# Performance work log

Hardware: AMD Instinct MI355X
Metric: run time of the kernel (lower is better)

## Reference

```python
import jax, jax.numpy as jnp
import numpy as np

DIM = 1024
HEADS = 16
DIM_HEAD = 64
INNER = HEADS * DIM_HEAD  # 1024
MLP = 4096
NQ = 16384
NW = 1024
LN_EPS = 1e-5
L2_EPS = 1e-12


def setup_inputs() -> dict:
    key = jax.random.key(0)
    ks = jax.random.split(key, 12)
    s = 0.02
    return {
        "queries": jax.random.normal(ks[0], (NQ, DIM), jnp.float32),
        "prototypes": jax.random.normal(ks[1], (NW, DIM), jnp.float32),
        "ln1_w": 1.0 + s * jax.random.normal(ks[2], (DIM,), jnp.float32),
        "ln1_b": s * jax.random.normal(ks[3], (DIM,), jnp.float32),
        "wq": s * jax.random.normal(ks[4], (DIM, INNER), jnp.float32),
        "wk": s * jax.random.normal(ks[5], (DIM, INNER), jnp.float32),
        "wv": s * jax.random.normal(ks[6], (DIM, INNER), jnp.float32),
        "wo": s * jax.random.normal(ks[7], (INNER, DIM), jnp.float32),
        "bo": jnp.zeros((DIM,), jnp.float32),
        "ln2_w": 1.0 + s * jax.random.normal(ks[8], (DIM,), jnp.float32),
        "ln2_b": s * jax.random.normal(ks[9], (DIM,), jnp.float32),
        "w1": s * jax.random.normal(ks[10], (DIM, MLP), jnp.float32),
        "b1": jnp.zeros((MLP,), jnp.float32),
        "w2": s * jax.random.normal(ks[11], (MLP, DIM), jnp.float32),
        "b2": jnp.zeros((DIM,), jnp.float32),
    }


def _layernorm(x, w, b):
    mu = jnp.mean(x, axis=-1, keepdims=True)
    var = jnp.mean(jnp.square(x - mu), axis=-1, keepdims=True)
    return (x - mu) * jax.lax.rsqrt(var + LN_EPS) * w + b


def _l2norm(x):
    n = jnp.sqrt(jnp.sum(jnp.square(x), axis=-1, keepdims=True))
    return x / jnp.maximum(n, L2_EPS)


def reference(queries, prototypes, ln1_w, ln1_b, wq, wk, wv, wo, bo,
              ln2_w, ln2_b, w1, b1, w2, b2):
    residual = queries
    qn = _layernorm(queries, ln1_w, ln1_b)
    pn = _layernorm(prototypes, ln1_w, ln1_b)
    # projections -> (h, q, d) / (h, n, d)
    q = (qn @ wq).reshape(NQ, HEADS, DIM_HEAD).transpose(1, 0, 2)
    k = (pn @ wk).reshape(NW, HEADS, DIM_HEAD).transpose(1, 0, 2)
    v = (pn @ wv).reshape(NW, HEADS, DIM_HEAD).transpose(1, 0, 2)
    attn = jnp.einsum('hqd,hnd->hqn', _l2norm(q), _l2norm(k))  # cosine, no softmax
    out = jnp.einsum('hqn,hnd->hqd', attn, v)
    out = out.transpose(1, 0, 2).reshape(NQ, INNER)
    out = out @ wo + bo + residual
    residual2 = out
    h = _layernorm(out, ln2_w, ln2_b)
    h = jax.nn.gelu(h @ w1 + b1, approximate=False) @ w2 + b2
    return h + residual2
```

## Files before the change

### kernel.cpp

```cpp
#include <hip/hip_runtime.h>
#include <hip/hip_bf16.h>

typedef _Float16 f16;
typedef __attribute__((ext_vector_type(8))) _Float16 f16x8;
typedef __attribute__((ext_vector_type(4))) _Float16 f16x4;
typedef __attribute__((ext_vector_type(4))) float f32x4;

#define DIM 1024
#define HEADS 16
#define DHEAD 64
#define MLPD 4096
#define NQ 16384
#define NW 1024
#define MCHUNK 32

#define WAITV(n) asm volatile("s_waitcnt vmcnt(" #n ")" ::: "memory")
#define WAITL0 asm volatile("s_waitcnt lgkmcnt(0)" ::: "memory")

__device__ __forceinline__ void glds16(const f16* g, f16* l) {
  __builtin_amdgcn_global_load_lds(
      (const __attribute__((address_space(1))) void*)g,
      (__attribute__((address_space(3))) void*)l, 16, 0, 0);
}

__global__ __launch_bounds__(256) void ln_f16_k(
    const float* __restrict__ X, const float* __restrict__ w,
    const float* __restrict__ b, f16* __restrict__ O) {
  const int row = blockIdx.x;
  const int t = threadIdx.x;
  const float4 v = ((const float4*)(X + (long)row * DIM))[t];
  float s = v.x + v.y + v.z + v.w;
  float s2 = v.x * v.x + v.y * v.y + v.z * v.z + v.w * v.w;
#pragma unroll
  for (int m = 1; m < 64; m <<= 1) {
    s += __shfl_xor(s, m);
    s2 += __shfl_xor(s2, m);
  }
  __shared__ float ps[4], ps2[4];
  const int lane = t & 63, wid = t >> 6;
  if (lane == 0) { ps[wid] = s; ps2[wid] = s2; }
  __syncthreads();
  s = ps[0] + ps[1] + ps[2] + ps[3];
  s2 = ps2[0] + ps2[1] + ps2[2] + ps2[3];
  const float mu = s * (1.0f / DIM);
  const float inv = rsqrtf(s2 * (1.0f / DIM) - mu * mu + 1e-5f);
  const float4 wv = ((const float4*)w)[t];
  const float4 bv = ((const float4*)b)[t];
  f16x4 o;
  o[0] = (f16)((v.x - mu) * inv * wv.x + bv.x);
  o[1] = (f16)((v.y - mu) * inv * wv.y + bv.y);
  o[2] = (f16)((v.z - mu) * inv * wv.z + bv.z);
  o[3] = (f16)((v.w - mu) * inv * wv.w + bv.w);
  *(f16x4*)(O + (long)row * DIM + t * 4) = o;
}

__global__ __launch_bounds__(256) void tcast_k(const float* __restrict__ X,
                                               f16* __restrict__ O, int R, int C) {
  __shared__ float tile[32][33];
  const int c0 = blockIdx.x * 32, r0 = blockIdx.y * 32;
  const int tx = threadIdx.x, ty = threadIdx.y;
#pragma unroll
  for (int j = 0; j < 4; ++j)
    tile[ty + j * 8][tx] = X[(long)(r0 + ty + j * 8) * C + c0 + tx];
  __syncthreads();
#pragma unroll
  for (int j = 0; j < 4; ++j)
    O[(long)(c0 + ty + j * 8) * R + r0 + tx] = (f16)tile[tx][ty + j * 8];
}

__global__ __launch_bounds__(256) void calc_m_part_k(const f16* __restrict__ kh,
                                                     const f16* __restrict__ v,
                                                     float* __restrict__ Mp) {
  const int h = blockIdx.x, ch = blockIdx.y;
  const int t = threadIdx.x;
  const int d1 = t >> 2;
  const int d2b = (t & 3) * 16;
  float acc[16] = {};
  const int n0 = ch * (NW / MCHUNK);
#pragma unroll 4
  for (int n = n0; n < n0 + NW / MCHUNK; ++n) {
    const float kv = (float)kh[(long)n * DIM + h * DHEAD + d1];
    const f16x8* vp = (const f16x8*)&v[(long)n * DIM + h * DHEAD + d2b];
    const f16x8 v0 = vp[0], v1 = vp[1];
#pragma unroll
    for (int j = 0; j < 8; ++j) acc[j] += kv * (float)v0[j];
#pragma unroll
    for (int j = 0; j < 8; ++j) acc[8 + j] += kv * (float)v1[j];
  }
  float* o = &Mp[((long)(h * MCHUNK + ch)) * 4096 + d1 * 64 + d2b];
#pragma unroll
  for (int j = 0; j < 16; ++j) o[j] = acc[j];
}

__global__ __launch_bounds__(256) void calc_m_reduce_k(const float* __restrict__ Mp,
                                                       float* __restrict__ Mo) {
  const int h = blockIdx.x;
  const int t = threadIdx.x;
#pragma unroll
  for (int e = t; e < 4096; e += 256) {
    float s = 0.f;
#pragma unroll
    for (int c = 0; c < MCHUNK; ++c)
      s += Mp[((long)(h * MCHUNK + c)) * 4096 + e];
    Mo[h * 4096 + e] = s;
  }
}

__global__ __launch_bounds__(256) void calc_wefft_k(const float* __restrict__ M,
                                                    const float* __restrict__ wo,
                                                    f16* __restrict__ Wt) {
  const int h = blockIdx.x, jt = blockIdx.y;
  const int t = threadIdx.x;
  const int jl = t & 63;
  const int il0 = (t >> 6) * 16;
  const int j = jt * 64 + jl;
  float acc[16] = {};
  for (int d = 0; d < DHEAD; ++d) {
    const float w = wo[(long)(h * DHEAD + d) * DIM + j];
    const float* mrow = &M[h * 4096 + il0 * 64 + d];
#pragma unroll
    for (int r = 0; r < 16; ++r) acc[r] += mrow[r * 64] * w;
  }
#pragma unroll
  for (int r = 0; r < 16; ++r)
    Wt[(long)j * DIM + h * DHEAD + il0 + r] = (f16)acc[r];
}

enum {
  EPI_F16 = 0,
  EPI_L2N = 1,
  EPI_BIAS_RES = 2,
  EPI_GELU = 3
};

template <int EPI>
__global__ __launch_bounds__(512, 2) void gemm256(
    const f16* __restrict__ A, const f16* __restrict__ Bt, int M, int N, int K,
    const float* __restrict__ bias, const float* resid, void* out) {
  __shared__ __align__(16) f16 lds[3 * 16384];

  const int tid = threadIdx.x;
  const int lane = tid & 63;
  const int wid = tid >> 6;
  const int wm = wid >> 2;
  const int wn = wid & 3;

  int bm, bn;
  {
    const int total = gridDim.x * gridDim.y;
    const int orig = blockIdx.y * gridDim.x + blockIdx.x;
    int swz = orig;
    if ((total & 7) == 0) swz = (orig & 7) * (total >> 3) + (orig >> 3);
    bm = swz % gridDim.x;
    bn = swz / gridDim.x;
  }

  const int srow = tid >> 2;
  const int scol = (((tid & 3) ^ ((tid >> 3) & 3))) * 8;
  const f16* agp = A + (long)(bm * 256 + srow) * K + scol;
  const f16* bgp = Bt + (long)(bn * 256 + srow) * K + scol;
  const long h128 = (long)128 * K;

  auto STAGE = [&](int c, int t) {
    const long go = (long)t * 32;
    f16* base = &lds[c * 16384 + tid * 8];
    glds16(agp + go, base);
    glds16(agp + h128 + go, base + 4096);
    glds16(bgp + go, base + 8192);
    glds16(bgp + h128 + go, base + 12288);
  };

  const int NT = K >> 5;
  STAGE(0, 0);
  STAGE(1, 1);
  STAGE(2, 2);
  WAITV(8);
  __builtin_amdgcn_s_barrier();

  const int l15 = lane & 15;
  const int kA = ((lane >> 4) * 8) ^ (((lane >> 1) & 3) * 8);
  const int abase = (wm * 128 + l15) * 32 + kA;
  const int bbase = (wn * 64 + l15) * 32 + kA;

  f32x4 acc[8][4] = {};

  for (int t = 0; t < NT; ++t) {
    const int c = t % 3;
    const f16* Ab = &lds[c * 16384];
    const f16* Bb = Ab + 8192;
    f16x8 a[8], b[4];
#pragma unroll
    for (int mi = 0; mi < 8; ++mi)
      a[mi] = *(const f16x8*)&Ab[abase + mi * 512];
#pragma unroll
    for (int nj = 0; nj < 4; ++nj)
      b[nj] = *(const f16x8*)&Bb[bbase + nj * 512];
    WAITL0;
    __builtin_amdgcn_sched_barrier(0);
    __builtin_amdgcn_s_barrier();
    if (t + 3 < NT) STAGE(c, t + 3);
    __builtin_amdgcn_s_setprio(1);
#pragma unroll
    for (int mi = 0; mi < 8; ++mi)
#pragma unroll
      for (int nj = 0; nj < 4; ++nj)
        acc[mi][nj] = __builtin_amdgcn_mfma_f32_16x16x32_f16(a[mi], b[nj],
                                                             acc[mi][nj], 0, 0, 0);
    __builtin_amdgcn_s_setprio(0);
    if (t + 4 <= NT) WAITV(8);
    else if (t + 3 == NT) WAITV(4);
    else if (t + 2 == NT) WAITV(0);
    __builtin_amdgcn_s_barrier();
  }

  const int r0 = bm * 256 + wm * 128;
  const int c0 = bn * 256 + wn * 64;
  const int lr = (lane >> 4) * 4;
  const int lc = l15;

#pragma unroll
  for (int mi = 0; mi < 8; ++mi) {
#pragma unroll
    for (int i = 0; i < 4; ++i) {
      const long r = r0 + mi * 16 + lr + i;
      if (EPI == EPI_L2N) {
        float ss = 0.f;
#pragma unroll
        for (int nj = 0; nj < 4; ++nj) {
          const float x = acc[mi][nj][i];
          ss += x * x;
        }
        ss += __shfl_xor(ss, 1);
        ss += __shfl_xor(ss, 2);
        ss += __shfl_xor(ss, 4);
        ss += __shfl_xor(ss, 8);
        const float inv = 1.0f / fmaxf(sqrtf(ss), 1e-12f);
#pragma unroll
        for (int nj = 0; nj < 4; ++nj)
          ((f16*)out)[r * N + c0 + nj * 16 + lc] = (f16)(acc[mi][nj][i] * inv);
      } else if (EPI == EPI_F16) {
#pragma unroll
        for (int nj = 0; nj < 4; ++nj)
          ((f16*)out)[r * N + c0 + nj * 16 + lc] = (f16)acc[mi][nj][i];
      } else if (EPI == EPI_BIAS_RES) {
#pragma unroll
        for (int nj = 0; nj < 4; ++nj) {
          const long c = c0 + nj * 16 + lc;
          ((float*)out)[r * N + c] = acc[mi][nj][i] + bias[c] + resid[r * N + c];
        }
      } else {
#pragma unroll
        for (int nj = 0; nj < 4; ++nj) {
          const long c = c0 + nj * 16 + lc;
          const float x = acc[mi][nj][i] + bias[c];
          ((f16*)out)[r * N + c] =
              (f16)(0.5f * x * (1.0f + erff(x * 0.70710678118654752f)));
        }
      }
    }
  }
}

extern "C" void kernel_launch(void* const* d_in, const int* in_sizes, int n_in,
                              void* d_out, int out_size, void* d_ws, size_t ws_size,
                              hipStream_t stream) {
  (void)in_sizes; (void)n_in; (void)out_size;
  const float* queries = (const float*)d_in[0];
  const float* prototypes = (const float*)d_in[1];
  const float* ln1_w = (const float*)d_in[2];
  const float* ln1_b = (const float*)d_in[3];
  const float* wq = (const float*)d_in[4];
  const float* wk = (const float*)d_in[5];
  const float* wv = (const float*)d_in[6];
  const float* wo = (const float*)d_in[7];
  const float* bo = (const float*)d_in[8];
  const float* ln2_w = (const float*)d_in[9];
  const float* ln2_b = (const float*)d_in[10];
  const float* w1 = (const float*)d_in[11];
  const float* b1 = (const float*)d_in[12];
  const float* w2 = (const float*)d_in[13];
  const float* b2 = (const float*)d_in[14];

  char* ws = (char*)d_ws;
  const size_t MB = 1024ull * 1024ull;
  if (ws_size < 176ull * MB) return;

  f16* QN = (f16*)(ws + 0);
  f16* QHAT = (f16*)(ws + 32 * MB);
  f16* PN = (f16*)(ws + 64 * MB);
  f16* WQT = (f16*)(ws + 66 * MB);
  f16* WKT = (f16*)(ws + 68 * MB);
  f16* WVT = (f16*)(ws + 70 * MB);
  f16* KHAT = (f16*)(ws + 72 * MB);
  f16* VBF = (f16*)(ws + 74 * MB);
  float* Mbuf = (float*)(ws + 76 * MB);
  f16* WEFFT = (f16*)(ws + 77 * MB);
  float* Mpart = (float*)(ws + 0);
  f16* G = (f16*)(ws + 0);
  f16* HBF = (f16*)(ws + 128 * MB);
  f16* W1T = (f16*)(ws + 160 * MB);
  f16* W2T = (f16*)(ws + 168 * MB);
  float* RES2 = (float*)d_out;

  ln_f16_k<<<NQ, 256, 0, stream>>>(queries, ln1_w, ln1_b, QN);
  ln_f16_k<<<NW, 256, 0, stream>>>(prototypes, ln1_w, ln1_b, PN);
  tcast_k<<<dim3(32, 32), dim3(32, 8), 0, stream>>>(wq, WQT, DIM, DIM);
  tcast_k<<<dim3(32, 32), dim3(32, 8), 0, stream>>>(wk, WKT, DIM, DIM);
  tcast_k<<<dim3(32, 32), dim3(32, 8), 0, stream>>>(wv, WVT, DIM, DIM);
  tcast_k<<<dim3(128, 32), dim3(32, 8), 0, stream>>>(w1, W1T, DIM, MLPD);
  tcast_k<<<dim3(32, 128), dim3(32, 8), 0, stream>>>(w2, W2T, MLPD, DIM);

  gemm256<EPI_L2N><<<dim3(NQ / 256, DIM / 256), 512, 0, stream>>>(
      QN, WQT, NQ, DIM, DIM, nullptr, nullptr, QHAT);
  gemm256<EPI_L2N><<<dim3(NW / 256, DIM / 256), 512, 0, stream>>>(
      PN, WKT, NW, DIM, DIM, nullptr, nullptr, KHAT);
  gemm256<EPI_F16><<<dim3(NW / 256, DIM / 256), 512, 0, stream>>>(
      PN, WVT, NW, DIM, DIM, nullptr, nullptr, VBF);

  calc_m_part_k<<<dim3(HEADS, MCHUNK), 256, 0, stream>>>(KHAT, VBF, Mpart);
  calc_m_reduce_k<<<HEADS, 256, 0, stream>>>(Mpart, Mbuf);
  calc_wefft_k<<<dim3(HEADS, 16), 256, 0, stream>>>(Mbuf, wo, WEFFT);

  gemm256<EPI_BIAS_RES><<<dim3(NQ / 256, DIM / 256), 512, 0, stream>>>(
      QHAT, WEFFT, NQ, DIM, DIM, bo, queries, RES2);

  ln_f16_k<<<NQ, 256, 0, stream>>>(RES2, ln2_w, ln2_b, HBF);

  gemm256<EPI_GELU><<<dim3(NQ / 256, MLPD / 256), 512, 0, stream>>>(
      HBF, W1T, NQ, MLPD, DIM, b1, nullptr, G);
  gemm256<EPI_BIAS_RES><<<dim3(NQ / 256, DIM / 256), 512, 0, stream>>>(
      G, W2T, NQ, DIM, MLPD, b2, RES2, (float*)d_out);
}
```

Before: 706.7 us.

## Restructure GEMM main loop into 4-phase ping-pong with interleaved half-tile loads

Replaces the 3-stage ring buffer (32-wide K tiles) with two 64-wide K buffers split into four phases. Each phase issues a quarter of the next tile's global-to-LDS loads and then runs half the MFMAs, so loads interleave more finely with compute. This raises LDS use to 128KB per block and adds more barriers per iteration. It also fixes a more intricate wait/barrier schedule that has to stay correct near the end of the K loop.

```diff
diff --git a/kernel.cpp b/kernel.cpp
--- a/kernel.cpp
+++ b/kernel.cpp
@@ -137,13 +137,14 @@
 __global__ __launch_bounds__(512, 2) void gemm256(
     const f16* __restrict__ A, const f16* __restrict__ Bt, int M, int N, int K,
     const float* __restrict__ bias, const float* resid, void* out) {
-  __shared__ __align__(16) f16 lds[3 * 16384];
+  __shared__ __align__(16) f16 lds[65536];
 
   const int tid = threadIdx.x;
   const int lane = tid & 63;
   const int wid = tid >> 6;
   const int wm = wid >> 2;
   const int wn = wid & 3;
+  const int l15 = lane & 15;
 
   int bm, bn;
   {
@@ -155,63 +156,98 @@
     bn = swz / gridDim.x;
   }
 
-  const int srow = tid >> 2;
-  const int scol = (((tid & 3) ^ ((tid >> 3) & 3))) * 8;
-  const f16* agp = A + (long)(bm * 256 + srow) * K + scol;
-  const f16* bgp = Bt + (long)(bn * 256 + srow) * K + scol;
-  const long h128 = (long)128 * K;
-
-  auto STAGE = [&](int c, int t) {
-    const long go = (long)t * 32;
-    f16* base = &lds[c * 16384 + tid * 8];
-    glds16(agp + go, base);
-    glds16(agp + h128 + go, base + 4096);
-    glds16(bgp + go, base + 8192);
-    glds16(bgp + h128 + go, base + 12288);
-  };
-
-  const int NT = K >> 5;
-  STAGE(0, 0);
-  STAGE(1, 1);
-  STAGE(2, 2);
+  const int scol8 = (((tid & 3) ^ ((tid >> 3) & 3))) * 8;
+  const f16* aSrc = A + (long)(bm * 256 + (tid >> 2)) * K + scol8;
+  const f16* bSrc = Bt + (long)(bn * 256 + (tid >> 2)) * K + scol8;
+  const long hK = (long)128 * K;
+  const int tid8 = tid * 8;
+
+  const int rslot8 = (((lane >> 4) ^ ((l15 >> 1) & 3))) * 8;
+  const int aRdBase = (wm * 128 + l15) * 32 + rslot8;
+  const int bRdBase = 16384 + (wn * 64 + l15) * 32 + rslot8;
+
+  f32x4 acc[8][4] = {};
+  const int NT = K >> 6;
+
+  glds16(aSrc, &lds[tid8]);
+  glds16(aSrc + hK, &lds[4096 + tid8]);
+  glds16(bSrc, &lds[16384 + tid8]);
+  glds16(bSrc + hK, &lds[16384 + 4096 + tid8]);
+  glds16(aSrc + 32, &lds[8192 + tid8]);
+  glds16(aSrc + hK + 32, &lds[8192 + 4096 + tid8]);
+  glds16(bSrc + 32, &lds[24576 + tid8]);
+  glds16(bSrc + hK + 32, &lds[24576 + 4096 + tid8]);
+  glds16(aSrc + 64, &lds[32768 + tid8]);
+  glds16(aSrc + hK + 64, &lds[32768 + 4096 + tid8]);
+  glds16(bSrc + 64, &lds[32768 + 16384 + tid8]);
+  glds16(bSrc + hK + 64, &lds[32768 + 16384 + 4096 + tid8]);
   WAITV(8);
   __builtin_amdgcn_s_barrier();
 
-  const int l15 = lane & 15;
-  const int kA = ((lane >> 4) * 8) ^ (((lane >> 1) & 3) * 8);
-  const int abase = (wm * 128 + l15) * 32 + kA;
-  const int bbase = (wn * 64 + l15) * 32 + kA;
-
-  f32x4 acc[8][4] = {};
-
-  for (int t = 0; t < NT; ++t) {
-    const int c = t % 3;
-    const f16* Ab = &lds[c * 16384];
-    const f16* Bb = Ab + 8192;
-    f16x8 a[8], b[4];
-#pragma unroll
-    for (int mi = 0; mi < 8; ++mi)
-      a[mi] = *(const f16x8*)&Ab[abase + mi * 512];
-#pragma unroll
-    for (int nj = 0; nj < 4; ++nj)
-      b[nj] = *(const f16x8*)&Bb[bbase + nj * 512];
-    WAITL0;
-    __builtin_amdgcn_sched_barrier(0);
+#define PHASE_CORE(KS, MH, LOADB)                                        \
+  {                                                                      \
+    const f16* Ap = L + (KS)*8192 + aRdBase + (MH)*2048;                 \
+    a[0] = *(const f16x8*)(Ap);                                          \
+    a[1] = *(const f16x8*)(Ap + 512);                                    \
+    a[2] = *(const f16x8*)(Ap + 1024);                                   \
+    a[3] = *(const f16x8*)(Ap + 1536);                                   \
+    if (LOADB) {                                                         \
+      const f16* Bp = L + (KS)*8192 + bRdBase;                           \
+      b[0] = *(const f16x8*)(Bp);                                        \
+      b[1] = *(const f16x8*)(Bp + 512);                                  \
+      b[2] = *(const f16x8*)(Bp + 1024);                                 \
+      b[3] = *(const f16x8*)(Bp + 1536);                                 \
+    }                                                                    \
+    __builtin_amdgcn_s_barrier();                                        \
+    WAITL0;                                                              \
+    __builtin_amdgcn_sched_barrier(0);                                   \
+    __builtin_amdgcn_s_setprio(1);                                       \
+    _Pragma("unroll") for (int j = 0; j < 4; ++j)                        \
+        _Pragma("unroll") for (int nj = 0; nj < 4; ++nj)                 \
+            acc[(MH)*4 + j][nj] = __builtin_amdgcn_mfma_f32_16x16x32_f16(\
+                a[j], b[nj], acc[(MH)*4 + j][nj], 0, 0, 0);              \
+    __builtin_amdgcn_s_setprio(0);                                       \
+  }
+
+  for (int g = 0; g < NT; ++g) {
+    f16* L = &lds[(g & 1) * 32768];
+    f16* Lo = &lds[((g & 1) ^ 1) * 32768];
+    const long ko1 = (long)(g + 1) * 64;
+    const long ko2 = (long)(g + 2) * 64;
+    const bool s1 = (g + 1) < NT, s2 = (g + 2) < NT;
+    f16x8 a[4], b[4];
+
+    if (s1) {
+      glds16(aSrc + ko1 + 32, Lo + 8192 + tid8);
+      glds16(aSrc + hK + ko1 + 32, Lo + 8192 + 4096 + tid8);
+    }
+    PHASE_CORE(0, 0, 1);
     __builtin_amdgcn_s_barrier();
-    if (t + 3 < NT) STAGE(c, t + 3);
-    __builtin_amdgcn_s_setprio(1);
-#pragma unroll
-    for (int mi = 0; mi < 8; ++mi)
-#pragma unroll
-      for (int nj = 0; nj < 4; ++nj)
-        acc[mi][nj] = __builtin_amdgcn_mfma_f32_16x16x32_f16(a[mi], b[nj],
-                                                             acc[mi][nj], 0, 0, 0);
-    __builtin_amdgcn_s_setprio(0);
-    if (t + 4 <= NT) WAITV(8);
-    else if (t + 3 == NT) WAITV(4);
-    else if (t + 2 == NT) WAITV(0);
+
+    if (s1) {
+      glds16(bSrc + ko1 + 32, Lo + 24576 + tid8);
+      glds16(bSrc + hK + ko1 + 32, Lo + 24576 + 4096 + tid8);
+    }
+    PHASE_CORE(0, 1, 0);
+    if (s1) { WAITV(8); } else { WAITV(0); }
     __builtin_amdgcn_s_barrier();
-  }
+
+    if (s2) {
+      glds16(aSrc + ko2, L + tid8);
+      glds16(aSrc + hK + ko2, L + 4096 + tid8);
+    }
+    PHASE_CORE(1, 0, 1);
+    __builtin_amdgcn_s_barrier();
+
+    if (s2) {
+      glds16(bSrc + ko2, L + 16384 + tid8);
+      glds16(bSrc + hK + ko2, L + 16384 + 4096 + tid8);
+    }
+    PHASE_CORE(1, 1, 0);
+    if (s2) { WAITV(8); } else if (s1) { WAITV(4); }
+    __builtin_amdgcn_s_barrier();
+  }
+#undef PHASE_CORE
 
   const int r0 = bm * 256 + wm * 128;
   const int c0 = bn * 256 + wn * 64;
```

Result: no change. 693.1 us (-1.9%).
